# Kernel optimization log

Measured on AMD Instinct MI355X. Metric: run time of the kernel, lower is better.

The kernel has to match this reference:

```python
import jax, jax.numpy as jnp
import numpy as np

B, L, WD = 4096, 30, 300          # batch of news, title length, word dim
H, AD = 20, 20                    # attention heads, per-head dim
MD = H * AD                       # multi_dim = 400
E, ED = 10, 100                   # entities per news, entity dim
QD = 200                          # query_vector_dim
CAT, CD = 18, 50                  # category vocab / dim
SUB, SD = 300, 50                 # subcategory vocab / dim


def _mha(x, wq, bq, wk, bk, wv, bv):
    # x: [B, L, Din] -> [B, L, MD]; standard multi-head self-attention
    b, l, _ = x.shape
    q = (x @ wq + bq).reshape(b, l, H, AD)
    k = (x @ wk + bk).reshape(b, l, H, AD)
    v = (x @ wv + bv).reshape(b, l, H, AD)
    scores = jnp.einsum('blhd,bmhd->bhlm', q, k) / jnp.sqrt(jnp.asarray(AD, x.dtype))
    attn = jax.nn.softmax(scores, axis=-1)
    out = jnp.einsum('bhlm,bmhd->blhd', attn, v)
    return out.reshape(b, l, MD)


def _layernorm(x, g, b):
    mu = jnp.mean(x, axis=-1, keepdims=True)
    var = jnp.var(x, axis=-1, keepdims=True)
    return (x - mu) / jnp.sqrt(var + 1e-5) * g + b


def _additive(x, w, b, q):
    # x: [B, L, D] -> [B, D]
    scores = jnp.tanh(x @ w + b) @ q            # [B, L]
    alpha = jax.nn.softmax(scores, axis=-1)
    return jnp.einsum('bl,bld->bd', alpha, x)


def setup_inputs() -> dict:
    key = jax.random.key(0)
    ks = iter(jax.random.split(key, 40))
    n = lambda shape, s=0.02: (jax.random.normal(next(ks), shape, dtype=jnp.float32) * s)
    inp = {
        'word_embedding': jax.random.normal(next(ks), (B, L, WD), dtype=jnp.float32),
        'entity_embedding': jax.random.normal(next(ks), (B, E, ED), dtype=jnp.float32),
        'category_index': jax.random.randint(next(ks), (B,), 0, CAT, dtype=jnp.int64 if jax.config.jax_enable_x64 else jnp.int32),
        'subcategory_index': jax.random.randint(next(ks), (B,), 0, SUB, dtype=jnp.int64 if jax.config.jax_enable_x64 else jnp.int32),
        # category / subcategory branches
        'emb_cat': n((CAT, CD), 1.0), 'fc1_w': n((CD, MD)), 'fc1_b': jnp.zeros((MD,), jnp.float32),
        'emb_sub': n((SUB, SD), 1.0), 'fc2_w': n((SD, MD)), 'fc2_b': jnp.zeros((MD,), jnp.float32),
        # word multi-head self-attention
        'wq': n((WD, MD)), 'bq': jnp.zeros((MD,), jnp.float32),
        'wk': n((WD, MD)), 'bk': jnp.zeros((MD,), jnp.float32),
        'wv': n((WD, MD)), 'bv': jnp.zeros((MD,), jnp.float32),
        # shared LayerNorm
        'ln_g': jnp.ones((MD,), jnp.float32), 'ln_b': jnp.zeros((MD,), jnp.float32),
        # word additive attention
        'wa_w': n((MD, QD)), 'wa_b': jnp.zeros((QD,), jnp.float32), 'wa_q': n((QD,), 1.0),
        # entity branch: fc3 + GCN (learnable adjacency over the E entities of a news)
        'fc3_w': n((ED, ED)), 'fc3_b': jnp.zeros((ED,), jnp.float32),
        'gcn_A': n((E, E), 1.0), 'gcn_w': n((ED, MD)), 'gcn_b': jnp.zeros((MD,), jnp.float32),
        'ea_w': n((MD, QD)), 'ea_b': jnp.zeros((QD,), jnp.float32), 'ea_q': n((QD,), 1.0),
        # final news-level additive attention over 4 views
        'na_w': n((MD, QD)), 'na_b': jnp.zeros((QD,), jnp.float32), 'na_q': n((QD,), 1.0),
    }
    return inp


def reference(word_embedding, entity_embedding, category_index, subcategory_index,
              emb_cat, fc1_w, fc1_b, emb_sub, fc2_w, fc2_b,
              wq, bq, wk, bk, wv, bv, ln_g, ln_b,
              wa_w, wa_b, wa_q, fc3_w, fc3_b, gcn_A, gcn_w, gcn_b,
              ea_w, ea_b, ea_q, na_w, na_b, na_q):
    # category / subcategory reps (dropout is identity in eval)
    cat_rep = jnp.tanh(emb_cat[category_index] @ fc1_w + fc1_b)      # [B, MD]
    sub_rep = jnp.tanh(emb_sub[subcategory_index] @ fc2_w + fc2_b)   # [B, MD]
    # word branch
    w = _mha(word_embedding, wq, bq, wk, bk, wv, bv)                 # [B, L, MD]
    w = _layernorm(w, ln_g, ln_b)
    word_rep = jnp.tanh(_additive(w, wa_w, wa_b, wa_q))              # [B, MD]
    # entity branch: fc3 -> intra-news GCN -> shared LayerNorm
    e = jnp.tanh(entity_embedding @ fc3_w + fc3_b)                   # [B, E, ED]
    e = jax.nn.relu(jnp.einsum('ef,bfd->bed', gcn_A, e) @ gcn_w + gcn_b)  # [B, E, MD]
    e = _layernorm(e, ln_g, ln_b)
    ent_rep = jnp.tanh(_additive(e, ea_w, ea_b, ea_q))               # [B, MD]
    # fuse the 4 views with additive attention
    views = jnp.stack([word_rep, ent_rep, cat_rep, sub_rep], axis=1)  # [B, 4, MD]
    news_rep = jnp.tanh(_additive(views, na_w, na_b, na_q))          # [B, MD]
    return news_rep
```

## Files before the change

### kernel.cpp

```cpp
#include <hip/hip_runtime.h>
#include <hip/hip_bf16.h>
#include <math.h>

#define B_  4096
#define L_  30
#define WD_ 300
#define H_  20
#define AD_ 20
#define MD_ 400
#define E_  10
#define ED_ 100
#define QD_ 200
#define CD_ 50
#define SD_ 50

typedef unsigned short ushort_t;
typedef __attribute__((ext_vector_type(8))) short bf16x8_t;
typedef __attribute__((ext_vector_type(4))) float f32x4_t;

#define SX_STR   328
#define QKV_STR  1218
#define OUTB_STR 424
#define SOUT_STR 401
#define P_STR    40
#define WT_K     320
#define WAT_K    416

#define N_WT    (1200 * WT_K)
#define N_WAT   (208 * WAT_K)
#define N_FC3T  (112 * 128)
#define N_GCNT  (400 * 128)
#define N_EAT   (208 * WAT_K)

union FragU {
  unsigned  u[4];
  short     s[8];
  bf16x8_t  h;
};

__device__ __forceinline__ ushort_t f2bf(float f) {
  unsigned u = __builtin_bit_cast(unsigned, f);
  unsigned r = (u + 0x7fffu + ((u >> 16) & 1u)) >> 16;
  return (ushort_t)r;
}
__device__ __forceinline__ float bf2f(ushort_t h) {
  return __builtin_bit_cast(float, ((unsigned)h) << 16);
}
__device__ __forceinline__ float wave_reduce_sum(float v) {
  #pragma unroll
  for (int off = 32; off > 0; off >>= 1) v += __shfl_xor(v, off);
  return v;
}
__device__ __forceinline__ void split2(float v, ushort_t* __restrict__ H,
                                       ushort_t* __restrict__ Lo, int idx) {
  const ushort_t h = f2bf(v);
  H[idx] = h;
  Lo[idx] = f2bf(v - bf2f(h));
}

__global__ __launch_bounds__(256) void prep_weights(
    const float* __restrict__ wq, const float* __restrict__ wk, const float* __restrict__ wv,
    const float* __restrict__ wa_w, const float* __restrict__ fc3_w,
    const float* __restrict__ gcn_w, const float* __restrict__ ea_w,
    ushort_t* __restrict__ Wt, ushort_t* __restrict__ Wat,
    ushort_t* __restrict__ fc3TH, ushort_t* __restrict__ fc3TL,
    ushort_t* __restrict__ gcnTH, ushort_t* __restrict__ gcnTL,
    ushort_t* __restrict__ eaTH, ushort_t* __restrict__ eaTL)
{
  int idx = blockIdx.x * 256 + threadIdx.x;
  if (idx < N_WT) {
    const int n = idx / WT_K, k = idx - n * WT_K;
    float v = 0.f;
    if (k < WD_) {
      const float* w = (n < 400) ? wq : (n < 800) ? wk : wv;
      const int c = (n < 400) ? n : (n < 800) ? n - 400 : n - 800;
      v = w[k * MD_ + c];
    }
    Wt[idx] = f2bf(v);
    return;
  }
  idx -= N_WT;
  if (idx < N_WAT) {
    const int q = idx / WAT_K, d = idx - q * WAT_K;
    Wat[idx] = (q < QD_ && d < MD_) ? f2bf(wa_w[d * QD_ + q]) : (ushort_t)0;
    return;
  }
  idx -= N_WAT;
  if (idx < N_FC3T) {
    const int n = idx / 128, k = idx - n * 128;
    const float v = (n < ED_ && k < ED_) ? fc3_w[k * ED_ + n] : 0.f;
    split2(v, fc3TH, fc3TL, idx);
    return;
  }
  idx -= N_FC3T;
  if (idx < N_GCNT) {
    const int n = idx / 128, k = idx - n * 128;
    const float v = (k < ED_) ? gcn_w[k * MD_ + n] : 0.f;
    split2(v, gcnTH, gcnTL, idx);
    return;
  }
  idx -= N_GCNT;
  if (idx < N_EAT) {
    const int q = idx / WAT_K, d = idx - q * WAT_K;
    const float v = (q < QD_ && d < MD_) ? ea_w[d * QD_ + q] : 0.f;
    split2(v, eaTH, eaTL, idx);
  }
}

__global__ __launch_bounds__(1024, 4) void word_branch_kernel(
    const float* __restrict__ X,
    const ushort_t* __restrict__ Wt, const ushort_t* __restrict__ Wat,
    const float* __restrict__ bq, const float* __restrict__ bk, const float* __restrict__ bv,
    const float* __restrict__ ln_g, const float* __restrict__ ln_b,
    const float* __restrict__ wa_b, const float* __restrict__ wa_q,
    float* __restrict__ word_rep)
{
  __shared__ __align__(16) union {
    ushort_t x[32 * SX_STR];
    ushort_t p[16 * 16 * P_STR];
  } uA;
  __shared__ __align__(16) union {
    ushort_t qkv[30 * QKV_STR];
    ushort_t o[32 * OUTB_STR];
  } uB;
  __shared__ __align__(16) float sOut[30 * SOUT_STR];
  __shared__ float sSc[32];
  __shared__ float sAlpha[32];

  const int b    = blockIdx.x;
  const int tid  = threadIdx.x;
  const int wave = tid >> 6;
  const int lane = tid & 63;
  const int lr   = lane & 15;
  const int kg   = lane >> 4;

  const float* xb = X + (size_t)b * (L_ * WD_);
  {
    const int r = tid >> 5;
    const int c0 = tid & 31;
    #pragma unroll
    for (int k = 0; k < 10; ++k) {
      const int c = c0 + k * 32;
      const float v = (r < L_ && c < WD_) ? xb[r * WD_ + c] : 0.f;
      uA.x[r * SX_STR + c] = f2bf(v);
    }
  }
  if (tid < 32) sSc[tid] = 0.f;
  __syncthreads();

  bf16x8_t axl[10], axh[10];
  #pragma unroll
  for (int ks = 0; ks < 10; ++ks) {
    axl[ks] = *reinterpret_cast<const bf16x8_t*>(&uA.x[lr * SX_STR + ks * 32 + kg * 8]);
    axh[ks] = *reinterpret_cast<const bf16x8_t*>(&uA.x[(16 + lr) * SX_STR + ks * 32 + kg * 8]);
  }
  for (int nt = wave; nt < 75; nt += 16) {
    const ushort_t* wbase = &Wt[(nt * 16 + lr) * WT_K + kg * 8];
    f32x4_t acc0 = {0,0,0,0}, acc1 = {0,0,0,0};
    #pragma unroll
    for (int ks = 0; ks < 10; ++ks) {
      bf16x8_t bf = *reinterpret_cast<const bf16x8_t*>(wbase + ks * 32);
      acc0 = __builtin_amdgcn_mfma_f32_16x16x32_bf16(axl[ks], bf, acc0, 0, 0, 0);
      acc1 = __builtin_amdgcn_mfma_f32_16x16x32_bf16(axh[ks], bf, acc1, 0, 0, 0);
    }
    const int col = nt * 16 + lr;
    const float bias = (col < 400) ? bq[col] : (col < 800) ? bk[col - 400] : bv[col - 800];
    #pragma unroll
    for (int i = 0; i < 4; ++i) {
      uB.qkv[(kg * 4 + i) * QKV_STR + col] = f2bf(acc0[i] + bias);
      const int r2 = 16 + kg * 4 + i;
      if (r2 < L_) uB.qkv[r2 * QKV_STR + col] = f2bf(acc1[i] + bias);
    }
  }
  __syncthreads();

  ushort_t* pw = &uA.p[wave * (16 * P_STR)];
  for (int u = wave; u < 2 * H_; u += 16) {
    const int h = u >> 1, mt = u & 1;
    const int hq = h * AD_, hk = 400 + h * AD_, hv = 800 + h * AD_;

    bf16x8_t aq, bkf[2];
    {
      FragU fq;
      fq.u[0]=fq.u[1]=fq.u[2]=fq.u[3]=0;
      const bool okrow = (mt == 0) || (lr < 14);
      if (okrow && kg < 3) {
        const ushort_t* pq = &uB.qkv[(mt * 16 + lr) * QKV_STR + hq + kg * 8];
        fq.u[0] = *(const unsigned*)(pq);     fq.u[1] = *(const unsigned*)(pq + 2);
        if (kg < 2) { fq.u[2] = *(const unsigned*)(pq + 4); fq.u[3] = *(const unsigned*)(pq + 6); }
      }
      aq = fq.h;
    }
    #pragma unroll
    for (int t = 0; t < 2; ++t) {
      FragU fk;
      fk.u[0]=fk.u[1]=fk.u[2]=fk.u[3]=0;
      const bool okrow = (t == 0) || (lr < 14);
      if (okrow && kg < 3) {
        const ushort_t* pk = &uB.qkv[(t * 16 + lr) * QKV_STR + hk + kg * 8];
        fk.u[0] = *(const unsigned*)(pk);     fk.u[1] = *(const unsigned*)(pk + 2);
        if (kg < 2) { fk.u[2] = *(const unsigned*)(pk + 4); fk.u[3] = *(const unsigned*)(pk + 6); }
      }
      bkf[t] = fk.h;
    }
    f32x4_t c0 = {0,0,0,0}, c1 = {0,0,0,0};
    c0 = __builtin_amdgcn_mfma_f32_16x16x32_bf16(aq, bkf[0], c0, 0, 0, 0);
    c1 = __builtin_amdgcn_mfma_f32_16x16x32_bf16(aq, bkf[1], c1, 0, 0, 0);

    const float SCALE = 0.2236067977499790f;
    #pragma unroll
    for (int i = 0; i < 4; ++i) {
      const float v0 = c0[i] * SCALE;
      const float v1 = (lr < 14) ? c1[i] * SCALE : -1e30f;
      float mx = fmaxf(v0, v1);
      mx = fmaxf(mx, __shfl_xor(mx, 1));
      mx = fmaxf(mx, __shfl_xor(mx, 2));
      mx = fmaxf(mx, __shfl_xor(mx, 4));
      mx = fmaxf(mx, __shfl_xor(mx, 8));
      const float e0 = __expf(v0 - mx);
      const float e1 = (lr < 14) ? __expf(v1 - mx) : 0.f;
      float s = e0 + e1;
      s += __shfl_xor(s, 1);
      s += __shfl_xor(s, 2);
      s += __shfl_xor(s, 4);
      s += __shfl_xor(s, 8);
      const float inv = 1.f / s;
      const int row = kg * 4 + i;
      pw[row * P_STR + lr]      = f2bf(e0 * inv);
      pw[row * P_STR + 16 + lr] = f2bf(e1 * inv);
    }
    __asm__ volatile("s_waitcnt lgkmcnt(0)" ::: "memory");

    bf16x8_t ap = *reinterpret_cast<const bf16x8_t*>(&pw[lr * P_STR + kg * 8]);
    bf16x8_t bvf[2];
    #pragma unroll
    for (int nt = 0; nt < 2; ++nt) {
      FragU f;
      const int d = nt * 16 + lr;
      if (d < AD_) {
        #pragma unroll
        for (int j = 0; j < 8; ++j) {
          const int rm = kg * 8 + j;
          f.s[j] = (rm < L_) ? (short)uB.qkv[rm * QKV_STR + hv + d] : (short)0;
        }
      } else {
        f.u[0]=f.u[1]=f.u[2]=f.u[3]=0;
      }
      bvf[nt] = f.h;
    }
    f32x4_t o0 = {0,0,0,0}, o1 = {0,0,0,0};
    o0 = __builtin_amdgcn_mfma_f32_16x16x32_bf16(ap, bvf[0], o0, 0, 0, 0);
    o1 = __builtin_amdgcn_mfma_f32_16x16x32_bf16(ap, bvf[1], o1, 0, 0, 0);

    #pragma unroll
    for (int nt = 0; nt < 2; ++nt) {
      const f32x4_t o = nt ? o1 : o0;
      const int d = nt * 16 + lr;
      if (d < AD_) {
        #pragma unroll
        for (int i = 0; i < 4; ++i) {
          const int r = mt * 16 + kg * 4 + i;
          if (r < L_) sOut[r * SOUT_STR + h * AD_ + d] = o[i];
        }
      }
    }
  }
  __syncthreads();

  for (int r = wave; r < L_; r += 16) {
    float s = 0.f, s2 = 0.f;
    for (int d = lane; d < MD_; d += 64) { const float v = sOut[r * SOUT_STR + d]; s += v; s2 += v * v; }
    s  = wave_reduce_sum(s);
    s2 = wave_reduce_sum(s2);
    const float mu  = s * (1.f / MD_);
    const float var = s2 * (1.f / MD_) - mu * mu;
    const float inv = rsqrtf(var + 1e-5f);
    for (int d = lane; d < MD_; d += 64) {
      const float nv = (sOut[r * SOUT_STR + d] - mu) * inv * ln_g[d] + ln_b[d];
      sOut[r * SOUT_STR + d] = nv;
      uB.o[r * OUTB_STR + d] = f2bf(nv);
    }
  }
  if (tid < 2 * 416) {
    const int r = 30 + (tid / 416), c = tid - (tid / 416) * 416;
    uB.o[r * OUTB_STR + c] = 0;
  }
  {
    const int id = tid;
    if (id < 30 * 16) {
      const int r = id >> 4, c = 400 + (id & 15);
      uB.o[r * OUTB_STR + c] = 0;
    }
  }
  __syncthreads();

  for (int t = wave; t < 26; t += 16) {
    const int mt = t & 1, nt = t >> 1;
    bf16x8_t afa[13];
    #pragma unroll
    for (int ks = 0; ks < 13; ++ks)
      afa[ks] = *reinterpret_cast<const bf16x8_t*>(&uB.o[(mt * 16 + lr) * OUTB_STR + ks * 32 + kg * 8]);
    const ushort_t* wbase = &Wat[(nt * 16 + lr) * WAT_K + kg * 8];
    f32x4_t acc = {0,0,0,0};
    #pragma unroll
    for (int ks = 0; ks < 13; ++ks) {
      bf16x8_t wf = *reinterpret_cast<const bf16x8_t*>(wbase + ks * 32);
      acc = __builtin_amdgcn_mfma_f32_16x16x32_bf16(afa[ks], wf, acc, 0, 0, 0);
    }
    const int q = nt * 16 + lr;
    if (q < QD_) {
      const float bb = wa_b[q], qq = wa_q[q];
      #pragma unroll
      for (int i = 0; i < 4; ++i) {
        const int row = mt * 16 + kg * 4 + i;
        if (row < L_) atomicAdd(&sSc[row], tanhf(acc[i] + bb) * qq);
      }
    }
  }
  __syncthreads();

  if (wave == 0) {
    const float v = (lane < L_) ? sSc[lane] : -1e30f;
    float mx = v;
    #pragma unroll
    for (int off = 32; off > 0; off >>= 1) mx = fmaxf(mx, __shfl_xor(mx, off));
    const float e = (lane < L_) ? __expf(v - mx) : 0.f;
    float s = e;
    #pragma unroll
    for (int off = 32; off > 0; off >>= 1) s += __shfl_xor(s, off);
    if (lane < L_) sAlpha[lane] = e / s;
  }
  __syncthreads();

  if (tid < MD_) {
    const int d = tid;
    float acc = 0.f;
    #pragma unroll 6
    for (int l = 0; l < L_; ++l) acc += sAlpha[l] * sOut[l * SOUT_STR + d];
    word_rep[(size_t)b * MD_ + d] = tanhf(acc);
  }
}

__global__ __launch_bounds__(512, 4) void entity_branch_kernel(
    const float* __restrict__ Ein,
    const ushort_t* __restrict__ fc3TH, const ushort_t* __restrict__ fc3TL,
    const float* __restrict__ fc3_b,
    const float* __restrict__ gcn_A,
    const ushort_t* __restrict__ gcnTH, const ushort_t* __restrict__ gcnTL,
    const float* __restrict__ gcn_b,
    const float* __restrict__ ln_g, const float* __restrict__ ln_b,
    const ushort_t* __restrict__ eaTH, const ushort_t* __restrict__ eaTL,
    const float* __restrict__ ea_b, const float* __restrict__ ea_q,
    float* __restrict__ ent_rep)
{
  __shared__ __align__(16) ushort_t sEh[16 * 136], sEl[16 * 136];
  __shared__ __align__(16) float    eF[E_ * 104];
  __shared__ __align__(16) ushort_t gH[16 * 136], gL[16 * 136];
  __shared__ __align__(16) float    sR[16 * SOUT_STR];
  __shared__ __align__(16) ushort_t oH[16 * OUTB_STR], oL[16 * OUTB_STR];
  __shared__ float sSc[16];
  __shared__ float sAlpha[16];

  const int b    = blockIdx.x;
  const int tid  = threadIdx.x;
  const int wave = tid >> 6;
  const int lane = tid & 63;
  const int lr   = lane & 15;
  const int kg   = lane >> 4;

  for (int id = tid; id < 16 * 128; id += 512) {
    const int r = id >> 7, c = id & 127;
    const float v = (r < E_ && c < ED_) ? Ein[(size_t)b * (E_ * ED_) + r * ED_ + c] : 0.f;
    const ushort_t hh = f2bf(v);
    sEh[r * 136 + c] = hh;
    sEl[r * 136 + c] = f2bf(v - bf2f(hh));
  }
  for (int id = tid; id < 16 * 136; id += 512) { gH[id] = 0; gL[id] = 0; }
  for (int id = tid; id < 16 * OUTB_STR; id += 512) { oH[id] = 0; oL[id] = 0; }
  if (tid < 16) sSc[tid] = 0.f;
  __syncthreads();

  for (int nt = wave; nt < 7; nt += 8) {
    f32x4_t acc = {0,0,0,0};
    #pragma unroll
    for (int ks = 0; ks < 4; ++ks) {
      const int kb = ks * 32 + kg * 8;
      bf16x8_t ah = *reinterpret_cast<const bf16x8_t*>(&sEh[lr * 136 + kb]);
      bf16x8_t al = *reinterpret_cast<const bf16x8_t*>(&sEl[lr * 136 + kb]);
      bf16x8_t wh = *reinterpret_cast<const bf16x8_t*>(&fc3TH[(nt * 16 + lr) * 128 + kb]);
      bf16x8_t wl = *reinterpret_cast<const bf16x8_t*>(&fc3TL[(nt * 16 + lr) * 128 + kb]);
      acc = __builtin_amdgcn_mfma_f32_16x16x32_bf16(ah, wh, acc, 0, 0, 0);
      acc = __builtin_amdgcn_mfma_f32_16x16x32_bf16(al, wh, acc, 0, 0, 0);
      acc = __builtin_amdgcn_mfma_f32_16x16x32_bf16(ah, wl, acc, 0, 0, 0);
    }
    const int d = nt * 16 + lr;
    if (d < ED_) {
      const float bias = fc3_b[d];
      #pragma unroll
      for (int i = 0; i < 4; ++i) {
        const int r = kg * 4 + i;
        if (r < E_) eF[r * 104 + d] = tanhf(acc[i] + bias);
      }
    }
  }
  __syncthreads();

  for (int id = tid; id < E_ * ED_; id += 512) {
    const int i = id / ED_, d = id - (id / ED_) * ED_;
    float acc = 0.f;
    #pragma unroll
    for (int f = 0; f < E_; ++f) acc += gcn_A[i * E_ + f] * eF[f * 104 + d];
    const ushort_t hh = f2bf(acc);
    gH[i * 136 + d] = hh;
    gL[i * 136 + d] = f2bf(acc - bf2f(hh));
  }
  __syncthreads();

  for (int nt = wave; nt < 25; nt += 8) {
    f32x4_t acc = {0,0,0,0};
    #pragma unroll
    for (int ks = 0; ks < 4; ++ks) {
      const int kb = ks * 32 + kg * 8;
      bf16x8_t ah = *reinterpret_cast<const bf16x8_t*>(&gH[lr * 136 + kb]);
      bf16x8_t al = *reinterpret_cast<const bf16x8_t*>(&gL[lr * 136 + kb]);
      bf16x8_t wh = *reinterpret_cast<const bf16x8_t*>(&gcnTH[(nt * 16 + lr) * 128 + kb]);
      bf16x8_t wl = *reinterpret_cast<const bf16x8_t*>(&gcnTL[(nt * 16 + lr) * 128 + kb]);
      acc = __builtin_amdgcn_mfma_f32_16x16x32_bf16(ah, wh, acc, 0, 0, 0);
      acc = __builtin_amdgcn_mfma_f32_16x16x32_bf16(al, wh, acc, 0, 0, 0);
      acc = __builtin_amdgcn_mfma_f32_16x16x32_bf16(ah, wl, acc, 0, 0, 0);
    }
    const int d = nt * 16 + lr;
    const float bias = gcn_b[d];
    #pragma unroll
    for (int i = 0; i < 4; ++i) {
      const int r = kg * 4 + i;
      if (r < E_) sR[r * SOUT_STR + d] = fmaxf(acc[i] + bias, 0.f);
    }
  }
  __syncthreads();

  for (int r = wave; r < E_; r += 8) {
    float s = 0.f, s2 = 0.f;
    for (int d = lane; d < MD_; d += 64) { const float v = sR[r * SOUT_STR + d]; s += v; s2 += v * v; }
    s  = wave_reduce_sum(s);
    s2 = wave_reduce_sum(s2);
    const float mu  = s * (1.f / MD_);
    const float var = s2 * (1.f / MD_) - mu * mu;
    const float inv = rsqrtf(var + 1e-5f);
    for (int d = lane; d < MD_; d += 64) {
      const float nv = (sR[r * SOUT_STR + d] - mu) * inv * ln_g[d] + ln_b[d];
      sR[r * SOUT_STR + d] = nv;
      const ushort_t hh = f2bf(nv);
      oH[r * OUTB_STR + d] = hh;
      oL[r * OUTB_STR + d] = f2bf(nv - bf2f(hh));
    }
  }
  __syncthreads();

  for (int nt = wave; nt < 13; nt += 8) {
    f32x4_t acc = {0,0,0,0};
    for (int ks = 0; ks < 13; ++ks) {
      const int kb = ks * 32 + kg * 8;
      bf16x8_t ah = *reinterpret_cast<const bf16x8_t*>(&oH[lr * OUTB_STR + kb]);
      bf16x8_t al = *reinterpret_cast<const bf16x8_t*>(&oL[lr * OUTB_STR + kb]);
      bf16x8_t wh = *reinterpret_cast<const bf16x8_t*>(&eaTH[(nt * 16 + lr) * WAT_K + kb]);
      bf16x8_t wl = *reinterpret_cast<const bf16x8_t*>(&eaTL[(nt * 16 + lr) * WAT_K + kb]);
      acc = __builtin_amdgcn_mfma_f32_16x16x32_bf16(ah, wh, acc, 0, 0, 0);
      acc = __builtin_amdgcn_mfma_f32_16x16x32_bf16(al, wh, acc, 0, 0, 0);
      acc = __builtin_amdgcn_mfma_f32_16x16x32_bf16(ah, wl, acc, 0, 0, 0);
    }
    const int q = nt * 16 + lr;
    if (q < QD_) {
      const float bb = ea_b[q], qq = ea_q[q];
      #pragma unroll
      for (int i = 0; i < 4; ++i) {
        const int r = kg * 4 + i;
        if (r < E_) atomicAdd(&sSc[r], tanhf(acc[i] + bb) * qq);
      }
    }
  }
  __syncthreads();

  if (wave == 0) {
    const float v = (lane < E_) ? sSc[lane] : -1e30f;
    float mx = v;
    #pragma unroll
    for (int off = 32; off > 0; off >>= 1) mx = fmaxf(mx, __shfl_xor(mx, off));
    const float e = (lane < E_) ? __expf(v - mx) : 0.f;
    float s = e;
    #pragma unroll
    for (int off = 32; off > 0; off >>= 1) s += __shfl_xor(s, off);
    if (lane < E_) sAlpha[lane] = e / s;
  }
  __syncthreads();

  if (tid < MD_) {
    const int d = tid;
    float acc = 0.f;
    #pragma unroll
    for (int i = 0; i < E_; ++i) acc += sAlpha[i] * sR[i * SOUT_STR + d];
    ent_rep[(size_t)b * MD_ + d] = tanhf(acc);
  }
}

__global__ __launch_bounds__(256) void catsub_kernel(
    const int* __restrict__ cat_idx, const int* __restrict__ sub_idx,
    const float* __restrict__ emb_cat, const float* __restrict__ fc1_w, const float* __restrict__ fc1_b,
    const float* __restrict__ emb_sub, const float* __restrict__ fc2_w, const float* __restrict__ fc2_b,
    float* __restrict__ cat_rep, float* __restrict__ sub_rep)
{
  int idx = blockIdx.x * 256 + threadIdx.x;
  const int total = B_ * MD_;
  if (idx < total) {
    const int b = idx / MD_, d = idx - (idx / MD_) * MD_;
    const float* row = emb_cat + (size_t)cat_idx[b] * CD_;
    float acc = fc1_b[d];
    #pragma unroll
    for (int k = 0; k < CD_; ++k) acc += row[k] * fc1_w[k * MD_ + d];
    cat_rep[idx] = tanhf(acc);
  } else {
    idx -= total;
    if (idx < total) {
      const int b = idx / MD_, d = idx - (idx / MD_) * MD_;
      const float* row = emb_sub + (size_t)sub_idx[b] * SD_;
      float acc = fc2_b[d];
      #pragma unroll
      for (int k = 0; k < SD_; ++k) acc += row[k] * fc2_w[k * MD_ + d];
      sub_rep[idx] = tanhf(acc);
    }
  }
}

__global__ __launch_bounds__(256) void fuse_kernel(
    const float* __restrict__ word_rep, const float* __restrict__ ent_rep,
    const float* __restrict__ cat_rep, const float* __restrict__ sub_rep,
    const float* __restrict__ na_w, const float* __restrict__ na_b, const float* __restrict__ na_q,
    float* __restrict__ out)
{
  __shared__ float sViews[4][MD_];
  __shared__ float sSc[4];
  __shared__ float sAlpha[4];
  const int b = blockIdx.x, tid = threadIdx.x;
  for (int d = tid; d < MD_; d += 256) {
    sViews[0][d] = word_rep[(size_t)b * MD_ + d];
    sViews[1][d] = ent_rep[(size_t)b * MD_ + d];
    sViews[2][d] = cat_rep[(size_t)b * MD_ + d];
    sViews[3][d] = sub_rep[(size_t)b * MD_ + d];
  }
  if (tid < 4) sSc[tid] = 0.f;
  __syncthreads();
  for (int id = tid; id < 4 * QD_; id += 256) {
    const int v = id / QD_, q = id - (id / QD_) * QD_;
    float acc = na_b[q];
    #pragma unroll 4
    for (int d = 0; d < MD_; ++d) acc += sViews[v][d] * na_w[d * QD_ + q];
    atomicAdd(&sSc[v], tanhf(acc) * na_q[q]);
  }
  __syncthreads();
  if (tid == 0) {
    float mx = -1e30f;
    for (int v = 0; v < 4; ++v) mx = fmaxf(mx, sSc[v]);
    float sum = 0.f;
    for (int v = 0; v < 4; ++v) { const float e = __expf(sSc[v] - mx); sAlpha[v] = e; sum += e; }
    const float inv = 1.f / sum;
    for (int v = 0; v < 4; ++v) sAlpha[v] *= inv;
  }
  __syncthreads();
  for (int d = tid; d < MD_; d += 256) {
    const float acc = sAlpha[0] * sViews[0][d] + sAlpha[1] * sViews[1][d] +
                      sAlpha[2] * sViews[2][d] + sAlpha[3] * sViews[3][d];
    out[(size_t)b * MD_ + d] = tanhf(acc);
  }
}

extern "C" void kernel_launch(void* const* d_in, const int* in_sizes, int n_in,
                              void* d_out, int out_size, void* d_ws, size_t ws_size,
                              hipStream_t stream) {
  const float* X        = (const float*)d_in[0];
  const float* Ein      = (const float*)d_in[1];
  const int*   cat_idx  = (const int*)d_in[2];
  const int*   sub_idx  = (const int*)d_in[3];
  const float* emb_cat  = (const float*)d_in[4];
  const float* fc1_w    = (const float*)d_in[5];
  const float* fc1_b    = (const float*)d_in[6];
  const float* emb_sub  = (const float*)d_in[7];
  const float* fc2_w    = (const float*)d_in[8];
  const float* fc2_b    = (const float*)d_in[9];
  const float* wq       = (const float*)d_in[10];
  const float* bq       = (const float*)d_in[11];
  const float* wk       = (const float*)d_in[12];
  const float* bk       = (const float*)d_in[13];
  const float* wv       = (const float*)d_in[14];
  const float* bv       = (const float*)d_in[15];
  const float* ln_g     = (const float*)d_in[16];
  const float* ln_b     = (const float*)d_in[17];
  const float* wa_w     = (const float*)d_in[18];
  const float* wa_b     = (const float*)d_in[19];
  const float* wa_q     = (const float*)d_in[20];
  const float* fc3_w    = (const float*)d_in[21];
  const float* fc3_b    = (const float*)d_in[22];
  const float* gcn_A    = (const float*)d_in[23];
  const float* gcn_w    = (const float*)d_in[24];
  const float* gcn_b    = (const float*)d_in[25];
  const float* ea_w     = (const float*)d_in[26];
  const float* ea_b     = (const float*)d_in[27];
  const float* ea_q     = (const float*)d_in[28];
  const float* na_w     = (const float*)d_in[29];
  const float* na_b     = (const float*)d_in[30];
  const float* na_q     = (const float*)d_in[31];

  float* out = (float*)d_out;
  const size_t BM = (size_t)B_ * MD_;
  float* word_rep = (float*)d_ws;
  float* ent_rep  = word_rep + BM;
  float* cat_rep  = ent_rep + BM;
  float* sub_rep  = cat_rep + BM;
  ushort_t* Wt    = (ushort_t*)(sub_rep + BM);
  ushort_t* Wat   = Wt + N_WT;
  ushort_t* fc3TH = Wat + N_WAT;
  ushort_t* fc3TL = fc3TH + N_FC3T;
  ushort_t* gcnTH = fc3TL + N_FC3T;
  ushort_t* gcnTL = gcnTH + N_GCNT;
  ushort_t* eaTH  = gcnTL + N_GCNT;
  ushort_t* eaTL  = eaTH + N_EAT;

  {
    const int total = N_WT + N_WAT + N_FC3T + N_GCNT + N_EAT;
    prep_weights<<<(total + 255) / 256, 256, 0, stream>>>(
        wq, wk, wv, wa_w, fc3_w, gcn_w, ea_w,
        Wt, Wat, fc3TH, fc3TL, gcnTH, gcnTL, eaTH, eaTL);
  }
  word_branch_kernel<<<B_, 1024, 0, stream>>>(X, Wt, Wat, bq, bk, bv,
                                              ln_g, ln_b, wa_b, wa_q, word_rep);
  entity_branch_kernel<<<B_, 512, 0, stream>>>(Ein, fc3TH, fc3TL, fc3_b, gcn_A,
                                               gcnTH, gcnTL, gcn_b,
                                               ln_g, ln_b, eaTH, eaTL, ea_b, ea_q, ent_rep);
  catsub_kernel<<<(2 * B_ * MD_) / 256, 256, 0, stream>>>(cat_idx, sub_idx,
                                                          emb_cat, fc1_w, fc1_b,
                                                          emb_sub, fc2_w, fc2_b,
                                                          cat_rep, sub_rep);
  fuse_kernel<<<B_, 256, 0, stream>>>(word_rep, ent_rep, cat_rep, sub_rep,
                                      na_w, na_b, na_q, out);
}
```

Before: 1.312 ms.

## Chunk word-branch QKV projection into four head-group passes to shrink LDS

The word-branch kernel now computes Q/K/V in four passes of five heads each, using a small per-pass QKV buffer instead of the full 30x1200 tile. The attention output and normalized activations are stored in bf16 rather than fp32, and the block size drops from 1024 to 768 threads. The aim is to cut shared-memory footprint so more blocks fit per CU and occupancy rises. In exchange, A fragments are reloaded from LDS every pass, some columns are recomputed across pass boundaries, there are extra barriers, and LayerNorm statistics lose precision from bf16 storage.

```diff
diff --git a/kernel.cpp b/kernel.cpp
--- a/kernel.cpp
+++ b/kernel.cpp
@@ -19,7 +19,8 @@
 typedef __attribute__((ext_vector_type(4))) float f32x4_t;
 
 #define SX_STR   328
-#define QKV_STR  1218
+#define QKVQ_STR 306
+#define SOB_STR  408
 #define OUTB_STR 424
 #define SOUT_STR 401
 #define P_STR    40
@@ -107,7 +108,7 @@
   }
 }
 
-__global__ __launch_bounds__(1024, 4) void word_branch_kernel(
+__global__ __launch_bounds__(768, 6) void word_branch_kernel(
     const float* __restrict__ X,
     const ushort_t* __restrict__ Wt, const ushort_t* __restrict__ Wat,
     const float* __restrict__ bq, const float* __restrict__ bk, const float* __restrict__ bv,
@@ -115,15 +116,10 @@
     const float* __restrict__ wa_b, const float* __restrict__ wa_q,
     float* __restrict__ word_rep)
 {
-  __shared__ __align__(16) union {
-    ushort_t x[32 * SX_STR];
-    ushort_t p[16 * 16 * P_STR];
-  } uA;
-  __shared__ __align__(16) union {
-    ushort_t qkv[30 * QKV_STR];
-    ushort_t o[32 * OUTB_STR];
-  } uB;
-  __shared__ __align__(16) float sOut[30 * SOUT_STR];
+  __shared__ __align__(16) ushort_t sX[32 * SX_STR];
+  __shared__ __align__(16) ushort_t qkvQ[30 * QKVQ_STR];
+  __shared__ __align__(16) ushort_t sOb[30 * SOB_STR];
+  __shared__ __align__(16) ushort_t pT[12 * 16 * P_STR];
   __shared__ float sSc[32];
   __shared__ float sAlpha[32];
 
@@ -135,171 +131,182 @@
   const int kg   = lane >> 4;
 
   const float* xb = X + (size_t)b * (L_ * WD_);
-  {
-    const int r = tid >> 5;
-    const int c0 = tid & 31;
-    #pragma unroll
-    for (int k = 0; k < 10; ++k) {
-      const int c = c0 + k * 32;
-      const float v = (r < L_ && c < WD_) ? xb[r * WD_ + c] : 0.f;
-      uA.x[r * SX_STR + c] = f2bf(v);
-    }
+  for (int idx = tid; idx < 32 * 320; idx += 768) {
+    const int r = idx / 320, c = idx - (idx / 320) * 320;
+    const float v = (r < L_ && c < WD_) ? xb[r * WD_ + c] : 0.f;
+    sX[r * SX_STR + c] = f2bf(v);
+  }
+  for (int id = tid; id < 30 * 8; id += 768) {
+    const int r = id >> 3, c = 400 + (id & 7);
+    sOb[r * SOB_STR + c] = 0;
   }
   if (tid < 32) sSc[tid] = 0.f;
   __syncthreads();
 
-  bf16x8_t axl[10], axh[10];
-  #pragma unroll
-  for (int ks = 0; ks < 10; ++ks) {
-    axl[ks] = *reinterpret_cast<const bf16x8_t*>(&uA.x[lr * SX_STR + ks * 32 + kg * 8]);
-    axh[ks] = *reinterpret_cast<const bf16x8_t*>(&uA.x[(16 + lr) * SX_STR + ks * 32 + kg * 8]);
-  }
-  for (int nt = wave; nt < 75; nt += 16) {
-    const ushort_t* wbase = &Wt[(nt * 16 + lr) * WT_K + kg * 8];
-    f32x4_t acc0 = {0,0,0,0}, acc1 = {0,0,0,0};
-    #pragma unroll
-    for (int ks = 0; ks < 10; ++ks) {
-      bf16x8_t bf = *reinterpret_cast<const bf16x8_t*>(wbase + ks * 32);
-      acc0 = __builtin_amdgcn_mfma_f32_16x16x32_bf16(axl[ks], bf, acc0, 0, 0, 0);
-      acc1 = __builtin_amdgcn_mfma_f32_16x16x32_bf16(axh[ks], bf, acc1, 0, 0, 0);
-    }
-    const int col = nt * 16 + lr;
-    const float bias = (col < 400) ? bq[col] : (col < 800) ? bk[col - 400] : bv[col - 800];
-    #pragma unroll
-    for (int i = 0; i < 4; ++i) {
-      uB.qkv[(kg * 4 + i) * QKV_STR + col] = f2bf(acc0[i] + bias);
-      const int r2 = 16 + kg * 4 + i;
-      if (r2 < L_) uB.qkv[r2 * QKV_STR + col] = f2bf(acc1[i] + bias);
-    }
-  }
-  __syncthreads();
-
-  ushort_t* pw = &uA.p[wave * (16 * P_STR)];
-  for (int u = wave; u < 2 * H_; u += 16) {
-    const int h = u >> 1, mt = u & 1;
-    const int hq = h * AD_, hk = 400 + h * AD_, hv = 800 + h * AD_;
-
-    bf16x8_t aq, bkf[2];
-    {
-      FragU fq;
-      fq.u[0]=fq.u[1]=fq.u[2]=fq.u[3]=0;
-      const bool okrow = (mt == 0) || (lr < 14);
-      if (okrow && kg < 3) {
-        const ushort_t* pq = &uB.qkv[(mt * 16 + lr) * QKV_STR + hq + kg * 8];
-        fq.u[0] = *(const unsigned*)(pq);     fq.u[1] = *(const unsigned*)(pq + 2);
-        if (kg < 2) { fq.u[2] = *(const unsigned*)(pq + 4); fq.u[3] = *(const unsigned*)(pq + 6); }
-      }
-      aq = fq.h;
-    }
-    #pragma unroll
-    for (int t = 0; t < 2; ++t) {
-      FragU fk;
-      fk.u[0]=fk.u[1]=fk.u[2]=fk.u[3]=0;
-      const bool okrow = (t == 0) || (lr < 14);
-      if (okrow && kg < 3) {
-        const ushort_t* pk = &uB.qkv[(t * 16 + lr) * QKV_STR + hk + kg * 8];
-        fk.u[0] = *(const unsigned*)(pk);     fk.u[1] = *(const unsigned*)(pk + 2);
-        if (kg < 2) { fk.u[2] = *(const unsigned*)(pk + 4); fk.u[3] = *(const unsigned*)(pk + 6); }
-      }
-      bkf[t] = fk.h;
-    }
-    f32x4_t c0 = {0,0,0,0}, c1 = {0,0,0,0};
-    c0 = __builtin_amdgcn_mfma_f32_16x16x32_bf16(aq, bkf[0], c0, 0, 0, 0);
-    c1 = __builtin_amdgcn_mfma_f32_16x16x32_bf16(aq, bkf[1], c1, 0, 0, 0);
-
-    const float SCALE = 0.2236067977499790f;
-    #pragma unroll
-    for (int i = 0; i < 4; ++i) {
-      const float v0 = c0[i] * SCALE;
-      const float v1 = (lr < 14) ? c1[i] * SCALE : -1e30f;
-      float mx = fmaxf(v0, v1);
-      mx = fmaxf(mx, __shfl_xor(mx, 1));
-      mx = fmaxf(mx, __shfl_xor(mx, 2));
-      mx = fmaxf(mx, __shfl_xor(mx, 4));
-      mx = fmaxf(mx, __shfl_xor(mx, 8));
-      const float e0 = __expf(v0 - mx);
-      const float e1 = (lr < 14) ? __expf(v1 - mx) : 0.f;
-      float s = e0 + e1;
-      s += __shfl_xor(s, 1);
-      s += __shfl_xor(s, 2);
-      s += __shfl_xor(s, 4);
-      s += __shfl_xor(s, 8);
-      const float inv = 1.f / s;
-      const int row = kg * 4 + i;
-      pw[row * P_STR + lr]      = f2bf(e0 * inv);
-      pw[row * P_STR + 16 + lr] = f2bf(e1 * inv);
-    }
-    __asm__ volatile("s_waitcnt lgkmcnt(0)" ::: "memory");
-
-    bf16x8_t ap = *reinterpret_cast<const bf16x8_t*>(&pw[lr * P_STR + kg * 8]);
-    bf16x8_t bvf[2];
-    #pragma unroll
-    for (int nt = 0; nt < 2; ++nt) {
-      FragU f;
-      const int d = nt * 16 + lr;
-      if (d < AD_) {
-        #pragma unroll
-        for (int j = 0; j < 8; ++j) {
-          const int rm = kg * 8 + j;
-          f.s[j] = (rm < L_) ? (short)uB.qkv[rm * QKV_STR + hv + d] : (short)0;
-        }
-      } else {
-        f.u[0]=f.u[1]=f.u[2]=f.u[3]=0;
-      }
-      bvf[nt] = f.h;
-    }
-    f32x4_t o0 = {0,0,0,0}, o1 = {0,0,0,0};
-    o0 = __builtin_amdgcn_mfma_f32_16x16x32_bf16(ap, bvf[0], o0, 0, 0, 0);
-    o1 = __builtin_amdgcn_mfma_f32_16x16x32_bf16(ap, bvf[1], o1, 0, 0, 0);
-
-    #pragma unroll
-    for (int nt = 0; nt < 2; ++nt) {
-      const f32x4_t o = nt ? o1 : o0;
-      const int d = nt * 16 + lr;
-      if (d < AD_) {
+  ushort_t* pw = &pT[wave * (16 * P_STR)];
+  #pragma unroll 1
+  for (int pass = 0; pass < 4; ++pass) {
+    const int qb = (100 * pass) & ~15;
+    const int p100 = 100 * pass;
+
+    for (int t = wave; t < 21; t += 12) {
+      const int sect = t / 7, ti = t - sect * 7;
+      const int gq = qb + ti * 16 + lr;
+      const int gcol = gq + ((sect == 0) ? 0 : (sect == 1) ? 400 : 800);
+      const ushort_t* wbase = &Wt[gcol * WT_K + kg * 8];
+      f32x4_t acc0 = {0,0,0,0}, acc1 = {0,0,0,0};
+      #pragma unroll
+      for (int ks = 0; ks < 10; ++ks) {
+        bf16x8_t bf  = *reinterpret_cast<const bf16x8_t*>(wbase + ks * 32);
+        bf16x8_t af0 = *reinterpret_cast<const bf16x8_t*>(&sX[lr * SX_STR + ks * 32 + kg * 8]);
+        bf16x8_t af1 = *reinterpret_cast<const bf16x8_t*>(&sX[(16 + lr) * SX_STR + ks * 32 + kg * 8]);
+        acc0 = __builtin_amdgcn_mfma_f32_16x16x32_bf16(af0, bf, acc0, 0, 0, 0);
+        acc1 = __builtin_amdgcn_mfma_f32_16x16x32_bf16(af1, bf, acc1, 0, 0, 0);
+      }
+      const float bias = (gcol < 400) ? bq[gcol] : (gcol < 800) ? bk[gcol - 400] : bv[gcol - 800];
+      const int lq = gq - p100;
+      if (lq >= 0 && lq < 100) {
+        const int lcol = sect * 102 + lq;
         #pragma unroll
         for (int i = 0; i < 4; ++i) {
-          const int r = mt * 16 + kg * 4 + i;
-          if (r < L_) sOut[r * SOUT_STR + h * AD_ + d] = o[i];
+          qkvQ[(kg * 4 + i) * QKVQ_STR + lcol] = f2bf(acc0[i] + bias);
+          const int r2 = 16 + kg * 4 + i;
+          if (r2 < L_) qkvQ[r2 * QKVQ_STR + lcol] = f2bf(acc1[i] + bias);
         }
       }
     }
-  }
-  __syncthreads();
-
-  for (int r = wave; r < L_; r += 16) {
+    __syncthreads();
+
+    for (int u = wave; u < 10; u += 12) {
+      const int hl = u >> 1, mt = u & 1;
+      const int h = pass * 5 + hl;
+      const int qloc = hl * 20, kloc = 102 + hl * 20, vloc = 204 + hl * 20;
+
+      bf16x8_t aq, bkf[2];
+      {
+        FragU fq;
+        fq.u[0]=fq.u[1]=fq.u[2]=fq.u[3]=0;
+        const bool okrow = (mt == 0) || (lr < 14);
+        if (okrow && kg < 3) {
+          const ushort_t* pq = &qkvQ[(mt * 16 + lr) * QKVQ_STR + qloc + kg * 8];
+          fq.u[0] = *(const unsigned*)(pq);     fq.u[1] = *(const unsigned*)(pq + 2);
+          if (kg < 2) { fq.u[2] = *(const unsigned*)(pq + 4); fq.u[3] = *(const unsigned*)(pq + 6); }
+        }
+        aq = fq.h;
+      }
+      #pragma unroll
+      for (int t = 0; t < 2; ++t) {
+        FragU fk;
+        fk.u[0]=fk.u[1]=fk.u[2]=fk.u[3]=0;
+        const bool okrow = (t == 0) || (lr < 14);
+        if (okrow && kg < 3) {
+          const ushort_t* pk = &qkvQ[(t * 16 + lr) * QKVQ_STR + kloc + kg * 8];
+          fk.u[0] = *(const unsigned*)(pk);     fk.u[1] = *(const unsigned*)(pk + 2);
+          if (kg < 2) { fk.u[2] = *(const unsigned*)(pk + 4); fk.u[3] = *(const unsigned*)(pk + 6); }
+        }
+        bkf[t] = fk.h;
+      }
+      f32x4_t c0 = {0,0,0,0}, c1 = {0,0,0,0};
+      c0 = __builtin_amdgcn_mfma_f32_16x16x32_bf16(aq, bkf[0], c0, 0, 0, 0);
+      c1 = __builtin_amdgcn_mfma_f32_16x16x32_bf16(aq, bkf[1], c1, 0, 0, 0);
+
+      const float SCALE = 0.2236067977499790f;
+      #pragma unroll
+      for (int i = 0; i < 4; ++i) {
+        const float v0 = c0[i] * SCALE;
+        const float v1 = (lr < 14) ? c1[i] * SCALE : -1e30f;
+        float mx = fmaxf(v0, v1);
+        mx = fmaxf(mx, __shfl_xor(mx, 1));
+        mx = fmaxf(mx, __shfl_xor(mx, 2));
+        mx = fmaxf(mx, __shfl_xor(mx, 4));
+        mx = fmaxf(mx, __shfl_xor(mx, 8));
+        const float e0 = __expf(v0 - mx);
+        const float e1 = (lr < 14) ? __expf(v1 - mx) : 0.f;
+        float s = e0 + e1;
+        s += __shfl_xor(s, 1);
+        s += __shfl_xor(s, 2);
+        s += __shfl_xor(s, 4);
+        s += __shfl_xor(s, 8);
+        const float inv = 1.f / s;
+        const int row = kg * 4 + i;
+        pw[row * P_STR + lr]      = f2bf(e0 * inv);
+        pw[row * P_STR + 16 + lr] = f2bf(e1 * inv);
+      }
+      __asm__ volatile("s_waitcnt lgkmcnt(0)" ::: "memory");
+
+      bf16x8_t ap = *reinterpret_cast<const bf16x8_t*>(&pw[lr * P_STR + kg * 8]);
+      bf16x8_t bvf[2];
+      #pragma unroll
+      for (int nt = 0; nt < 2; ++nt) {
+        FragU f;
+        const int d = nt * 16 + lr;
+        if (d < AD_) {
+          #pragma unroll
+          for (int j = 0; j < 8; ++j) {
+            const int rm = kg * 8 + j;
+            f.s[j] = (rm < L_) ? (short)qkvQ[rm * QKVQ_STR + vloc + d] : (short)0;
+          }
+        } else {
+          f.u[0]=f.u[1]=f.u[2]=f.u[3]=0;
+        }
+        bvf[nt] = f.h;
+      }
+      f32x4_t o0 = {0,0,0,0}, o1 = {0,0,0,0};
+      o0 = __builtin_amdgcn_mfma_f32_16x16x32_bf16(ap, bvf[0], o0, 0, 0, 0);
+      o1 = __builtin_amdgcn_mfma_f32_16x16x32_bf16(ap, bvf[1], o1, 0, 0, 0);
+
+      #pragma unroll
+      for (int nt = 0; nt < 2; ++nt) {
+        const f32x4_t o = nt ? o1 : o0;
+        const int d = nt * 16 + lr;
+        if (d < AD_) {
+          #pragma unroll
+          for (int i = 0; i < 4; ++i) {
+            const int r = mt * 16 + kg * 4 + i;
+            if (r < L_) sOb[r * SOB_STR + h * AD_ + d] = f2bf(o[i]);
+          }
+        }
+      }
+    }
+    __syncthreads();
+  }
+
+  for (int r = wave; r < L_; r += 12) {
     float s = 0.f, s2 = 0.f;
-    for (int d = lane; d < MD_; d += 64) { const float v = sOut[r * SOUT_STR + d]; s += v; s2 += v * v; }
+    #pragma unroll
+    for (int j = 0; j < 7; ++j) {
+      const int d = lane + j * 64;
+      if (d < MD_) { const float v = bf2f(sOb[r * SOB_STR + d]); s += v; s2 += v * v; }
+    }
     s  = wave_reduce_sum(s);
     s2 = wave_reduce_sum(s2);
     const float mu  = s * (1.f / MD_);
     const float var = s2 * (1.f / MD_) - mu * mu;
     const float inv = rsqrtf(var + 1e-5f);
-    for (int d = lane; d < MD_; d += 64) {
-      const float nv = (sOut[r * SOUT_STR + d] - mu) * inv * ln_g[d] + ln_b[d];
-      sOut[r * SOUT_STR + d] = nv;
-      uB.o[r * OUTB_STR + d] = f2bf(nv);
-    }
-  }
-  if (tid < 2 * 416) {
-    const int r = 30 + (tid / 416), c = tid - (tid / 416) * 416;
-    uB.o[r * OUTB_STR + c] = 0;
-  }
-  {
-    const int id = tid;
-    if (id < 30 * 16) {
-      const int r = id >> 4, c = 400 + (id & 15);
-      uB.o[r * OUTB_STR + c] = 0;
-    }
-  }
-  __syncthreads();
-
-  for (int t = wave; t < 26; t += 16) {
+    #pragma unroll
+    for (int j = 0; j < 7; ++j) {
+      const int d = lane + j * 64;
+      if (d < MD_) {
+        const float nv = (bf2f(sOb[r * SOB_STR + d]) - mu) * inv * ln_g[d] + ln_b[d];
+        sOb[r * SOB_STR + d] = f2bf(nv);
+      }
+    }
+  }
+  __syncthreads();
+
+  for (int t = wave; t < 26; t += 12) {
     const int mt = t & 1, nt = t >> 1;
+    const int row = mt * 16 + lr;
+    const bool okrow = row < L_;
     bf16x8_t afa[13];
     #pragma unroll
-    for (int ks = 0; ks < 13; ++ks)
-      afa[ks] = *reinterpret_cast<const bf16x8_t*>(&uB.o[(mt * 16 + lr) * OUTB_STR + ks * 32 + kg * 8]);
+    for (int ks = 0; ks < 13; ++ks) {
+      if (okrow && !(ks == 12 && kg == 3)) {
+        afa[ks] = *reinterpret_cast<const bf16x8_t*>(&sOb[row * SOB_STR + ks * 32 + kg * 8]);
+      } else {
+        FragU z; z.u[0]=z.u[1]=z.u[2]=z.u[3]=0; afa[ks] = z.h;
+      }
+    }
     const ushort_t* wbase = &Wat[(nt * 16 + lr) * WAT_K + kg * 8];
     f32x4_t acc = {0,0,0,0};
     #pragma unroll
@@ -312,8 +319,8 @@
       const float bb = wa_b[q], qq = wa_q[q];
       #pragma unroll
       for (int i = 0; i < 4; ++i) {
-        const int row = mt * 16 + kg * 4 + i;
-        if (row < L_) atomicAdd(&sSc[row], tanhf(acc[i] + bb) * qq);
+        const int rr = mt * 16 + kg * 4 + i;
+        if (rr < L_) atomicAdd(&sSc[rr], tanhf(acc[i] + bb) * qq);
       }
     }
   }
@@ -336,7 +343,7 @@
     const int d = tid;
     float acc = 0.f;
     #pragma unroll 6
-    for (int l = 0; l < L_; ++l) acc += sAlpha[l] * sOut[l * SOUT_STR + d];
+    for (int l = 0; l < L_; ++l) acc += sAlpha[l] * bf2f(sOb[l * SOB_STR + d]);
     word_rep[(size_t)b * MD_ + d] = tanhf(acc);
   }
 }
@@ -630,8 +637,8 @@
         wq, wk, wv, wa_w, fc3_w, gcn_w, ea_w,
         Wt, Wat, fc3TH, fc3TL, gcnTH, gcnTL, eaTH, eaTL);
   }
-  word_branch_kernel<<<B_, 1024, 0, stream>>>(X, Wt, Wat, bq, bk, bv,
-                                              ln_g, ln_b, wa_b, wa_q, word_rep);
+  word_branch_kernel<<<B_, 768, 0, stream>>>(X, Wt, Wat, bq, bk, bv,
+                                             ln_g, ln_b, wa_b, wa_q, word_rep);
   entity_branch_kernel<<<B_, 512, 0, stream>>>(Ein, fc3TH, fc3TL, fc3_b, gcn_A,
                                                gcnTH, gcnTL, gcn_b,
                                                ln_g, ln_b, eaTH, eaTL, ea_b, ea_q, ent_rep);
```

After: 1.855 ms. 41.3% more time.
